# Optimization experiments

Hardware: AMD Instinct MI355X
Metric: run time of the kernel (lower is better)

The kernel has to match this reference:

```python
import jax, jax.numpy as jnp
import numpy as np

N = 8192
FEAT = 3
TRIG = 2
SA = 2
H = 64
ACT = 3
NEG = -1.0e9
EPS = 1e-5


def setup_inputs() -> dict:
    key = jax.random.key(0)
    ks = jax.random.split(key, 24)
    s = 0.05
    node_features = jax.random.uniform(ks[0], (N, FEAT), dtype=jnp.float32)
    adj = jax.random.randint(ks[1], (N, N), 0, 2).astype(jnp.float32)
    # ensure self-loops so every row has at least one neighbor
    adj_matrix = jnp.maximum(adj, jnp.eye(N, dtype=jnp.float32))
    trigger_context = jax.random.uniform(ks[2], (TRIG,), dtype=jnp.float32)
    sa_priors = jax.random.normal(ks[3], (N, SA), dtype=jnp.float32)
    p = lambda k, sh: jax.random.normal(k, sh, dtype=jnp.float32) * s
    return {
        "node_features": node_features,
        "adj_matrix": adj_matrix,
        "trigger_context": trigger_context,
        "sa_priors": sa_priors,
        # node_encoder: Linear(5,64) -> ReLU -> Linear(64,64)
        "w1": p(ks[4], (FEAT + TRIG, H)), "b1": jnp.zeros((H,), jnp.float32),
        "w2": p(ks[5], (H, H)), "b2": jnp.zeros((H,), jnp.float32),
        "wq": p(ks[6], (H, H)), "bq": jnp.zeros((H,), jnp.float32),
        "wk": p(ks[7], (H, H)), "bk": jnp.zeros((H,), jnp.float32),
        "wg": p(ks[8], (TRIG, H)), "bg": jnp.zeros((H,), jnp.float32),
        "stateful_bias": jnp.zeros((1,), jnp.float32),
        "wm": p(ks[9], (H, H)), "bm": jnp.zeros((H,), jnp.float32),
        "ln_g": jnp.ones((H,), jnp.float32), "ln_b": jnp.zeros((H,), jnp.float32),
        "wa1": p(ks[10], (H + SA, H)), "ba1": jnp.zeros((H,), jnp.float32),
        "wa2": p(ks[11], (H, ACT)), "ba2": jnp.zeros((ACT,), jnp.float32),
    }


def reference(node_features, adj_matrix, trigger_context, sa_priors,
              w1, b1, w2, b2, wq, bq, wk, bk, wg, bg, stateful_bias,
              wm, bm, ln_g, ln_b, wa1, ba1, wa2, ba2):
    n = node_features.shape[0]
    trig = jnp.broadcast_to(trigger_context[None, :], (n, TRIG))
    x = jnp.concatenate([node_features, trig], axis=1)          # [N, 5]
    h = jax.nn.relu(x @ w1 + b1) @ w2 + b2                       # [N, H]
    q = h @ wq + bq
    k = h @ wk + bk
    scores = (q @ k.T) * (1.0 / np.sqrt(H))                      # [N, N]
    gate_factor = jnp.mean(jax.nn.sigmoid(trigger_context @ wg + bg))
    topo = jnp.where(adj_matrix == 0, jnp.float32(NEG), adj_matrix)
    is_stateful = node_features[:, 2]
    is_reactive = 1.0 - trigger_context[0]
    sb = jnp.outer(is_stateful, is_stateful) * (stateful_bias[0] * is_reactive)
    scores = scores * gate_factor + topo + sb
    attn = jax.nn.softmax(scores, axis=1)                        # [N, N]
    messages = h @ wm + bm
    aggregated = attn @ messages                                 # [N, H]
    z = h + aggregated
    mu = jnp.mean(z, axis=-1, keepdims=True)
    var = jnp.mean(jnp.square(z - mu), axis=-1, keepdims=True)
    emb = (z - mu) * jax.lax.rsqrt(var + EPS) * ln_g + ln_b      # LayerNorm
    ai = jnp.concatenate([emb, sa_priors], axis=1)               # [N, H+2]
    q_values = jax.nn.relu(ai @ wa1 + ba1) @ wa2 + ba2           # [N, 3]
    return q_values
```

## Files before the change

kernel.cpp:

```cpp
#include <hip/hip_runtime.h>
#include <hip/hip_bf16.h>
#include <math.h>

#define N 8192
#define EPSV 1e-05f
#define NSPLIT 16
#define CPS (N / NSPLIT)
#define NTILE (CPS / 64)

typedef short bf16x8 __attribute__((ext_vector_type(8)));
typedef float f32x4 __attribute__((ext_vector_type(4)));
typedef float f32x16 __attribute__((ext_vector_type(16)));
typedef unsigned short u16;
typedef unsigned int u32;

#define WS_SCAL 0
#define WS_H    64
#define WS_ST   (WS_H + N * 64)
#define WS_SBI  (WS_ST + N)
#define WS_DEN  (WS_SBI + N)
#define WS_AGG  (WS_DEN + N)
#define WS_F_END (WS_AGG + N * 64)
#define WU_BASE (WS_F_END * 2)
#define WU_QB (WU_BASE)
#define WU_KB (WU_BASE + N * 64)
#define WU_MB (WU_BASE + 2 * N * 64)
#define WU_MT (WU_BASE + 3 * N * 64)

static __device__ __forceinline__ u16 f2bf(float f) {
    __hip_bfloat16 h = __float2bfloat16(f);
    return *(u16*)&h;
}
static __device__ __forceinline__ u32 pk2(float a, float b) {
    return (u32)f2bf(a) | ((u32)f2bf(b) << 16);
}
static __device__ __forceinline__ bf16x8 mk8(u32 a, u32 b, u32 c, u32 d) {
    union { u32 u[4]; bf16x8 v; } x;
    x.u[0] = a; x.u[1] = b; x.u[2] = c; x.u[3] = d;
    return x.v;
}

#define TILE_BARRIER() asm volatile("s_waitcnt lgkmcnt(0)\n\ts_barrier" ::: "memory")

__global__ void prep_k(const float* __restrict__ tc, const float* __restrict__ wg,
                       const float* __restrict__ bg, const float* __restrict__ sbias,
                       float* __restrict__ scal) {
    int j = threadIdx.x;
    float v = tc[0] * wg[j] + tc[1] * wg[64 + j] + bg[j];
    float g = 1.0f / (1.0f + __expf(-v));
    for (int off = 32; off; off >>= 1) g += __shfl_xor(g, off, 64);
    if (j == 0) {
        scal[0] = 0.125f * (g * (1.0f / 64.0f));
        scal[1] = sbias[0] * (1.0f - tc[0]);
    }
}

__global__ __launch_bounds__(256) void embed_k(
    const float* __restrict__ nf, const float* __restrict__ tc,
    const float* __restrict__ w1, const float* __restrict__ b1,
    const float* __restrict__ w2, const float* __restrict__ b2,
    const float* __restrict__ wq, const float* __restrict__ bq,
    const float* __restrict__ wk, const float* __restrict__ bk,
    const float* __restrict__ wm, const float* __restrict__ bm,
    float* __restrict__ ws)
{
    const int w = threadIdx.x >> 6, lane = threadIdx.x & 63;
    const int row = blockIdx.x * 4 + w;
    __shared__ float ts[4][64], hs[4][64];
    const float qscale = ws[WS_SCAL + 0];
    const float coef   = ws[WS_SCAL + 1];
    const float f0 = nf[row * 3], f1 = nf[row * 3 + 1], f2 = nf[row * 3 + 2];
    const float t0 = tc[0], t1 = tc[1];
    ws[WS_AGG + (size_t)row * 64 + lane] = 0.0f;
    float v = b1[lane];
    v = fmaf(f0, w1[lane], v);
    v = fmaf(f1, w1[64 + lane], v);
    v = fmaf(f2, w1[128 + lane], v);
    v = fmaf(t0, w1[192 + lane], v);
    v = fmaf(t1, w1[256 + lane], v);
    ts[w][lane] = fmaxf(v, 0.0f);
    __syncthreads();
    float hv = b2[lane];
    #pragma unroll 8
    for (int j = 0; j < 64; j++) hv = fmaf(ts[w][j], w2[j * 64 + lane], hv);
    hs[w][lane] = hv;
    ws[WS_H + row * 64 + lane] = hv;
    __syncthreads();
    float qv = bq[lane], kv = bk[lane], mv = bm[lane];
    #pragma unroll 4
    for (int j = 0; j < 64; j++) {
        const float hj = hs[w][j];
        qv = fmaf(hj, wq[j * 64 + lane], qv);
        kv = fmaf(hj, wk[j * 64 + lane], kv);
        mv = fmaf(hj, wm[j * 64 + lane], mv);
    }
    u16* wu = (u16*)ws;
    wu[WU_QB + row * 64 + lane] = f2bf(qv * qscale);
    wu[WU_KB + row * 64 + lane] = f2bf(kv);
    wu[WU_MB + row * 64 + lane] = f2bf(mv);
    if (lane == 0) {
        ws[WS_ST + row]  = f2;
        ws[WS_SBI + row] = f2 * coef;
        ws[WS_DEN + row] = 0.0f;
    }
}

__global__ __launch_bounds__(256) void transp_k(float* __restrict__ ws) {
    const u16* mb = (const u16*)ws + WU_MB;
    u16* mt = (u16*)ws + WU_MT;
    __shared__ __align__(16) u16 tile[64][72];
    const int i0 = blockIdx.x * 64;
    const int t = threadIdx.x;
    {
        const int r = t >> 2, cb = (t & 3) * 16;
        *(uint4*)&tile[r][cb]     = *(const uint4*)&mb[(size_t)(i0 + r) * 64 + cb];
        *(uint4*)&tile[r][cb + 8] = *(const uint4*)&mb[(size_t)(i0 + r) * 64 + cb + 8];
    }
    __syncthreads();
    const int c = t >> 2, rb = (t & 3) * 16;
    u16 tmp[16];
    #pragma unroll
    for (int i = 0; i < 16; i++) tmp[i] = tile[rb + i][c];
    *(uint4*)&mt[(size_t)c * N + i0 + rb]     = *(uint4*)&tmp[0];
    *(uint4*)&mt[(size_t)c * N + i0 + rb + 8] = *(uint4*)&tmp[8];
}

__global__ __launch_bounds__(256, 3) void attn_k(const float* __restrict__ adj,
                                                 float* __restrict__ ws)
{
    const int rb = blockIdx.x, sp = blockIdx.y;
    const int i0 = rb * 128, j0 = sp * CPS;
    const int tid = threadIdx.x;
    const int w = tid >> 6, lane = tid & 63;
    const int hi = lane >> 5, l31 = lane & 31;

    __shared__ __align__(16) u16 ks[2][64][68];
    __shared__ __align__(16) u16 ms[2][64][68];
    __shared__ float stl[CPS];

    const u16* qb  = (const u16*)ws + WU_QB;
    const u16* kbp = (const u16*)ws + WU_KB;
    const u16* mtp = (const u16*)ws + WU_MT;

    const int sr = tid >> 2, scb = (tid & 3) * 16;

    *(uint4*)&ks[0][sr][scb]     = *(const uint4*)&kbp[(size_t)(j0 + sr) * 64 + scb];
    *(uint4*)&ks[0][sr][scb + 8] = *(const uint4*)&kbp[(size_t)(j0 + sr) * 64 + scb + 8];
    *(uint4*)&ms[0][sr][scb]     = *(const uint4*)&mtp[(size_t)sr * N + j0 + scb];
    *(uint4*)&ms[0][sr][scb + 8] = *(const uint4*)&mtp[(size_t)sr * N + j0 + scb + 8];
    stl[tid]       = ws[WS_ST + j0 + tid];
    stl[tid + 256] = ws[WS_ST + j0 + tid + 256];
    __syncthreads();

    const int qrow = i0 + w * 32 + l31;
    const u16* qr = qb + (size_t)qrow * 64;
    bf16x8 qf[4];
    #pragma unroll
    for (int s = 0; s < 4; s++) qf[s] = *(const bf16x8*)&qr[s * 16 + hi * 8];

    const float sbr = ws[WS_SBI + qrow];
    const float* adjr = adj + (size_t)qrow * N;

    f32x16 acc[2];
    #pragma unroll
    for (int hb = 0; hb < 2; hb++)
        #pragma unroll
        for (int i = 0; i < 16; i++) acc[hb][i] = 0.0f;
    float den = 0.0f;

    f32x4 av[4];
    #pragma unroll
    for (int c2 = 0; c2 < 4; c2++)
        av[c2] = *(const f32x4*)&adjr[j0 + c2 * 8 + hi * 4];

    uint4 rk0, rk1, rm0, rm1;

    for (int t = 0; t < NTILE; t++) {
        const int cur = t & 1;
        #pragma unroll
        for (int kb = 0; kb < 2; kb++) {
            const int colb = j0 + t * 64 + kb * 32;
            const int loc  = t * 64 + kb * 32;

            if (kb == 0 && t + 1 < NTILE) {
                const int jn = j0 + (t + 1) * 64;
                rk0 = *(const uint4*)&kbp[(size_t)(jn + sr) * 64 + scb];
                rk1 = *(const uint4*)&kbp[(size_t)(jn + sr) * 64 + scb + 8];
                rm0 = *(const uint4*)&mtp[(size_t)sr * N + jn + scb];
                rm1 = *(const uint4*)&mtp[(size_t)sr * N + jn + scb + 8];
            }

            const bool pn = (2 * t + kb + 1 < 2 * NTILE);
            f32x4 avn[4];
            if (pn) {
                #pragma unroll
                for (int c2 = 0; c2 < 4; c2++)
                    avn[c2] = *(const f32x4*)&adjr[colb + 32 + c2 * 8 + hi * 4];
            } else {
                #pragma unroll
                for (int c2 = 0; c2 < 4; c2++) avn[c2] = av[c2];
            }

            f32x16 d;
            #pragma unroll
            for (int i = 0; i < 16; i++) d[i] = 0.0f;
            #pragma unroll
            for (int s = 0; s < 4; s++) {
                const bf16x8 kf = *(const bf16x8*)&ks[cur][kb * 32 + l31][s * 16 + hi * 8];
                d = __builtin_amdgcn_mfma_f32_32x32x16_bf16(kf, qf[s], d, 0, 0, 0);
            }

            u32 wlo[4], whi[4];
            #pragma unroll
            for (int c2 = 0; c2 < 4; c2++) {
                const f32x4 sv = *(const f32x4*)&stl[loc + c2 * 8 + hi * 4];
                const f32x4 a4 = av[c2];
                const float p0 = a4[0] * __expf(fmaf(sbr, sv[0], d[c2 * 4 + 0]));
                const float p1 = a4[1] * __expf(fmaf(sbr, sv[1], d[c2 * 4 + 1]));
                const float p2 = a4[2] * __expf(fmaf(sbr, sv[2], d[c2 * 4 + 2]));
                const float p3 = a4[3] * __expf(fmaf(sbr, sv[3], d[c2 * 4 + 3]));
                den += (p0 + p1) + (p2 + p3);
                wlo[c2] = pk2(p0, p1);
                whi[c2] = pk2(p2, p3);
            }

            bf16x8 pa[2];
            #pragma unroll
            for (int s2 = 0; s2 < 2; s2++) {
                const u32 xl0 = (u32)__shfl_xor((int)wlo[2 * s2],     32, 64);
                const u32 xh0 = (u32)__shfl_xor((int)whi[2 * s2],     32, 64);
                const u32 xl1 = (u32)__shfl_xor((int)wlo[2 * s2 + 1], 32, 64);
                const u32 xh1 = (u32)__shfl_xor((int)whi[2 * s2 + 1], 32, 64);
                const u32 f0 = hi ? xl1 : wlo[2 * s2];
                const u32 f1 = hi ? xh1 : whi[2 * s2];
                const u32 f2 = hi ? wlo[2 * s2 + 1] : xl0;
                const u32 f3 = hi ? whi[2 * s2 + 1] : xh0;
                pa[s2] = mk8(f0, f1, f2, f3);
            }

            #pragma unroll
            for (int hb = 0; hb < 2; hb++) {
                #pragma unroll
                for (int s2 = 0; s2 < 2; s2++) {
                    const bf16x8 mf = *(const bf16x8*)
                        &ms[cur][hb * 32 + l31][kb * 32 + s2 * 16 + hi * 8];
                    acc[hb] = __builtin_amdgcn_mfma_f32_32x32x16_bf16(pa[s2], mf, acc[hb], 0, 0, 0);
                }
            }

            if (kb == 1 && t + 1 < NTILE) {
                *(uint4*)&ks[cur ^ 1][sr][scb]     = rk0;
                *(uint4*)&ks[cur ^ 1][sr][scb + 8] = rk1;
                *(uint4*)&ms[cur ^ 1][sr][scb]     = rm0;
                *(uint4*)&ms[cur ^ 1][sr][scb + 8] = rm1;
            }

            #pragma unroll
            for (int c2 = 0; c2 < 4; c2++) av[c2] = avn[c2];
        }
        if (t + 1 < NTILE) TILE_BARRIER();
    }

    float* aggp = ws + WS_AGG;
    #pragma unroll
    for (int hb = 0; hb < 2; hb++) {
        #pragma unroll
        for (int reg = 0; reg < 16; reg++) {
            const int qv = (reg & 3) + 8 * (reg >> 2) + 4 * hi;
            unsafeAtomicAdd(&aggp[(size_t)(i0 + w * 32 + qv) * 64 + hb * 32 + l31],
                            acc[hb][reg]);
        }
    }
    den += __shfl_xor(den, 32, 64);
    if (hi == 0) unsafeAtomicAdd(&ws[WS_DEN + i0 + w * 32 + l31], den);
}

__global__ __launch_bounds__(256) void final_k(
    const float* __restrict__ sa, const float* __restrict__ ln_g,
    const float* __restrict__ ln_b,
    const float* __restrict__ wa1, const float* __restrict__ ba1,
    const float* __restrict__ wa2, const float* __restrict__ ba2,
    const float* __restrict__ ws, float* __restrict__ out)
{
    const int w = threadIdx.x >> 6, lane = threadIdx.x & 63;
    const int row = blockIdx.x * 4 + w;
    __shared__ float es[4][64], hs2[4][64];
    const float a = ws[WS_AGG + (size_t)row * 64 + lane];
    const float d = ws[WS_DEN + row];
    const float z = ws[WS_H + row * 64 + lane] + a / d;
    float mu = z;
    for (int off = 32; off; off >>= 1) mu += __shfl_xor(mu, off, 64);
    mu *= (1.0f / 64.0f);
    const float zc = z - mu;
    float var = zc * zc;
    for (int off = 32; off; off >>= 1) var += __shfl_xor(var, off, 64);
    var *= (1.0f / 64.0f);
    const float emb = zc * rsqrtf(var + EPSV) * ln_g[lane] + ln_b[lane];
    es[w][lane] = emb;
    __syncthreads();
    const float sa0 = sa[row * 2], sa1 = sa[row * 2 + 1];
    float hv = ba1[lane];
    #pragma unroll 8
    for (int c = 0; c < 64; c++) hv = fmaf(es[w][c], wa1[c * 64 + lane], hv);
    hv = fmaf(sa0, wa1[64 * 64 + lane], hv);
    hv = fmaf(sa1, wa1[65 * 64 + lane], hv);
    hs2[w][lane] = fmaxf(hv, 0.0f);
    __syncthreads();
    if (lane < 3) {
        float o = ba2[lane];
        for (int u = 0; u < 64; u++) o = fmaf(hs2[w][u], wa2[u * 3 + lane], o);
        out[row * 3 + lane] = o;
    }
}

extern "C" void kernel_launch(void* const* d_in, const int* in_sizes, int n_in,
                              void* d_out, int out_size, void* d_ws, size_t ws_size,
                              hipStream_t stream)
{
    const float* nf  = (const float*)d_in[0];
    const float* adj = (const float*)d_in[1];
    const float* tc  = (const float*)d_in[2];
    const float* sa  = (const float*)d_in[3];
    const float* w1  = (const float*)d_in[4];
    const float* b1  = (const float*)d_in[5];
    const float* w2  = (const float*)d_in[6];
    const float* b2  = (const float*)d_in[7];
    const float* wq  = (const float*)d_in[8];
    const float* bq  = (const float*)d_in[9];
    const float* wk  = (const float*)d_in[10];
    const float* bk  = (const float*)d_in[11];
    const float* wg  = (const float*)d_in[12];
    const float* bg  = (const float*)d_in[13];
    const float* sb  = (const float*)d_in[14];
    const float* wm  = (const float*)d_in[15];
    const float* bm  = (const float*)d_in[16];
    const float* lng = (const float*)d_in[17];
    const float* lnb = (const float*)d_in[18];
    const float* wa1 = (const float*)d_in[19];
    const float* ba1 = (const float*)d_in[20];
    const float* wa2 = (const float*)d_in[21];
    const float* ba2 = (const float*)d_in[22];
    float* ws  = (float*)d_ws;
    float* out = (float*)d_out;

    prep_k<<<1, 64, 0, stream>>>(tc, wg, bg, sb, ws + WS_SCAL);
    embed_k<<<N / 4, 256, 0, stream>>>(nf, tc, w1, b1, w2, b2, wq, bq, wk, bk,
                                       wm, bm, ws);
    transp_k<<<N / 64, 256, 0, stream>>>(ws);
    attn_k<<<dim3(N / 128, NSPLIT), 256, 0, stream>>>(adj, ws);
    final_k<<<N / 4, 256, 0, stream>>>(sa, lng, lnb, wa1, ba1, wa2, ba2, ws, out);
}
```

Measured before the change: 471.0 us.

## Transpose score MFMA output and stage probabilities through LDS instead of shuffles

Swaps the MFMA operand order so each lane holds one key column across 16 query rows. Adjacency loads become scalar per-row loads that are coalesced across lanes. Probabilities are written to a per-wave LDS tile and read back as bf16x8 operands, which replaces the cross-half shuffle repacking. The denominator is now reduced across lanes at the end. The costs are 16 scalar adj loads per step instead of four vector loads, extra LDS traffic, and higher register use for den and sbir, which may hurt occupancy.

```diff
diff --git a/kernel.cpp b/kernel.cpp
--- a/kernel.cpp
+++ b/kernel.cpp
@@ -30,14 +30,6 @@
 static __device__ __forceinline__ u16 f2bf(float f) {
     __hip_bfloat16 h = __float2bfloat16(f);
     return *(u16*)&h;
-}
-static __device__ __forceinline__ u32 pk2(float a, float b) {
-    return (u32)f2bf(a) | ((u32)f2bf(b) << 16);
-}
-static __device__ __forceinline__ bf16x8 mk8(u32 a, u32 b, u32 c, u32 d) {
-    union { u32 u[4]; bf16x8 v; } x;
-    x.u[0] = a; x.u[1] = b; x.u[2] = c; x.u[3] = d;
-    return x.v;
 }
 
 #define TILE_BARRIER() asm volatile("s_waitcnt lgkmcnt(0)\n\ts_barrier" ::: "memory")
@@ -136,6 +128,7 @@
 
     __shared__ __align__(16) u16 ks[2][64][68];
     __shared__ __align__(16) u16 ms[2][64][68];
+    __shared__ __align__(16) u16 ps[4][32][40];
     __shared__ float stl[CPS];
 
     const u16* qb  = (const u16*)ws + WU_QB;
@@ -152,26 +145,37 @@
     stl[tid + 256] = ws[WS_ST + j0 + tid + 256];
     __syncthreads();
 
-    const int qrow = i0 + w * 32 + l31;
-    const u16* qr = qb + (size_t)qrow * 64;
+    const int q0 = i0 + w * 32;
+
+    const u16* qr = qb + (size_t)(q0 + l31) * 64;
     bf16x8 qf[4];
     #pragma unroll
     for (int s = 0; s < 4; s++) qf[s] = *(const bf16x8*)&qr[s * 16 + hi * 8];
 
-    const float sbr = ws[WS_SBI + qrow];
-    const float* adjr = adj + (size_t)qrow * N;
+    float sbir[16];
+    #pragma unroll
+    for (int r = 0; r < 16; r++) {
+        const int qv = (r & 3) + 8 * (r >> 2) + 4 * hi;
+        sbir[r] = ws[WS_SBI + q0 + qv];
+    }
 
     f32x16 acc[2];
     #pragma unroll
     for (int hb = 0; hb < 2; hb++)
         #pragma unroll
         for (int i = 0; i < 16; i++) acc[hb][i] = 0.0f;
-    float den = 0.0f;
-
-    f32x4 av[4];
-    #pragma unroll
-    for (int c2 = 0; c2 < 4; c2++)
-        av[c2] = *(const f32x4*)&adjr[j0 + c2 * 8 + hi * 4];
+    float den[16];
+    #pragma unroll
+    for (int r = 0; r < 16; r++) den[r] = 0.0f;
+
+    const float* adjh = adj + (size_t)(q0 + 4 * hi) * N + j0 + l31;
+
+    float ac[16], an[16];
+    #pragma unroll
+    for (int r = 0; r < 16; r++) {
+        const int cr = (r & 3) + 8 * (r >> 2);
+        ac[r] = adjh[(size_t)cr * N];
+    }
 
     uint4 rk0, rk1, rm0, rm1;
 
@@ -179,8 +183,7 @@
         const int cur = t & 1;
         #pragma unroll
         for (int kb = 0; kb < 2; kb++) {
-            const int colb = j0 + t * 64 + kb * 32;
-            const int loc  = t * 64 + kb * 32;
+            const int loc = t * 64 + kb * 32;
 
             if (kb == 0 && t + 1 < NTILE) {
                 const int jn = j0 + (t + 1) * 64;
@@ -190,15 +193,15 @@
                 rm1 = *(const uint4*)&mtp[(size_t)sr * N + jn + scb + 8];
             }
 
-            const bool pn = (2 * t + kb + 1 < 2 * NTILE);
-            f32x4 avn[4];
-            if (pn) {
+            if (loc + 32 < CPS) {
                 #pragma unroll
-                for (int c2 = 0; c2 < 4; c2++)
-                    avn[c2] = *(const f32x4*)&adjr[colb + 32 + c2 * 8 + hi * 4];
+                for (int r = 0; r < 16; r++) {
+                    const int cr = (r & 3) + 8 * (r >> 2);
+                    an[r] = adjh[(size_t)cr * N + loc + 32];
+                }
             } else {
                 #pragma unroll
-                for (int c2 = 0; c2 < 4; c2++) avn[c2] = av[c2];
+                for (int r = 0; r < 16; r++) an[r] = ac[r];
             }
 
             f32x16 d;
@@ -207,44 +210,26 @@
             #pragma unroll
             for (int s = 0; s < 4; s++) {
                 const bf16x8 kf = *(const bf16x8*)&ks[cur][kb * 32 + l31][s * 16 + hi * 8];
-                d = __builtin_amdgcn_mfma_f32_32x32x16_bf16(kf, qf[s], d, 0, 0, 0);
-            }
-
-            u32 wlo[4], whi[4];
-            #pragma unroll
-            for (int c2 = 0; c2 < 4; c2++) {
-                const f32x4 sv = *(const f32x4*)&stl[loc + c2 * 8 + hi * 4];
-                const f32x4 a4 = av[c2];
-                const float p0 = a4[0] * __expf(fmaf(sbr, sv[0], d[c2 * 4 + 0]));
-                const float p1 = a4[1] * __expf(fmaf(sbr, sv[1], d[c2 * 4 + 1]));
-                const float p2 = a4[2] * __expf(fmaf(sbr, sv[2], d[c2 * 4 + 2]));
-                const float p3 = a4[3] * __expf(fmaf(sbr, sv[3], d[c2 * 4 + 3]));
-                den += (p0 + p1) + (p2 + p3);
-                wlo[c2] = pk2(p0, p1);
-                whi[c2] = pk2(p2, p3);
-            }
-
-            bf16x8 pa[2];
+                d = __builtin_amdgcn_mfma_f32_32x32x16_bf16(qf[s], kf, d, 0, 0, 0);
+            }
+
+            const float stc = stl[loc + l31];
+            #pragma unroll
+            for (int r = 0; r < 16; r++) {
+                const int qv = (r & 3) + 8 * (r >> 2) + 4 * hi;
+                const float p = ac[r] * __expf(fmaf(sbir[r], stc, d[r]));
+                den[r] += p;
+                ps[w][qv][l31] = f2bf(p);
+            }
+
             #pragma unroll
             for (int s2 = 0; s2 < 2; s2++) {
-                const u32 xl0 = (u32)__shfl_xor((int)wlo[2 * s2],     32, 64);
-                const u32 xh0 = (u32)__shfl_xor((int)whi[2 * s2],     32, 64);
-                const u32 xl1 = (u32)__shfl_xor((int)wlo[2 * s2 + 1], 32, 64);
-                const u32 xh1 = (u32)__shfl_xor((int)whi[2 * s2 + 1], 32, 64);
-                const u32 f0 = hi ? xl1 : wlo[2 * s2];
-                const u32 f1 = hi ? xh1 : whi[2 * s2];
-                const u32 f2 = hi ? wlo[2 * s2 + 1] : xl0;
-                const u32 f3 = hi ? whi[2 * s2 + 1] : xh0;
-                pa[s2] = mk8(f0, f1, f2, f3);
-            }
-
-            #pragma unroll
-            for (int hb = 0; hb < 2; hb++) {
+                const bf16x8 pa = *(const bf16x8*)&ps[w][l31][s2 * 16 + hi * 8];
                 #pragma unroll
-                for (int s2 = 0; s2 < 2; s2++) {
+                for (int hb = 0; hb < 2; hb++) {
                     const bf16x8 mf = *(const bf16x8*)
                         &ms[cur][hb * 32 + l31][kb * 32 + s2 * 16 + hi * 8];
-                    acc[hb] = __builtin_amdgcn_mfma_f32_32x32x16_bf16(pa[s2], mf, acc[hb], 0, 0, 0);
+                    acc[hb] = __builtin_amdgcn_mfma_f32_32x32x16_bf16(pa, mf, acc[hb], 0, 0, 0);
                 }
             }
 
@@ -256,23 +241,39 @@
             }
 
             #pragma unroll
-            for (int c2 = 0; c2 < 4; c2++) av[c2] = avn[c2];
+            for (int r = 0; r < 16; r++) ac[r] = an[r];
         }
         if (t + 1 < NTILE) TILE_BARRIER();
     }
 
+    #pragma unroll
+    for (int r = 0; r < 16; r++) {
+        float dv = den[r];
+        dv += __shfl_xor(dv, 1, 64);
+        dv += __shfl_xor(dv, 2, 64);
+        dv += __shfl_xor(dv, 4, 64);
+        dv += __shfl_xor(dv, 8, 64);
+        dv += __shfl_xor(dv, 16, 64);
+        den[r] = dv;
+    }
+    if (l31 == 0) {
+        #pragma unroll
+        for (int r = 0; r < 16; r++) {
+            const int qv = (r & 3) + 8 * (r >> 2) + 4 * hi;
+            unsafeAtomicAdd(&ws[WS_DEN + q0 + qv], den[r]);
+        }
+    }
+
     float* aggp = ws + WS_AGG;
     #pragma unroll
     for (int hb = 0; hb < 2; hb++) {
         #pragma unroll
-        for (int reg = 0; reg < 16; reg++) {
-            const int qv = (reg & 3) + 8 * (reg >> 2) + 4 * hi;
-            unsafeAtomicAdd(&aggp[(size_t)(i0 + w * 32 + qv) * 64 + hb * 32 + l31],
-                            acc[hb][reg]);
+        for (int r = 0; r < 16; r++) {
+            const int qv = (r & 3) + 8 * (r >> 2) + 4 * hi;
+            unsafeAtomicAdd(&aggp[(size_t)(q0 + qv) * 64 + hb * 32 + l31],
+                            acc[hb][r]);
         }
     }
-    den += __shfl_xor(den, 32, 64);
-    if (hi == 0) unsafeAtomicAdd(&ws[WS_DEN + i0 + w * 32 + l31], den);
 }
 
 __global__ __launch_bounds__(256) void final_k(
```

Result: no change. 474.5 us (+0.8%).

## Pre-pack Q/K/M into MFMA fragment layout and drop LDS staging in attention

Applied to the files above, without the earlier changes.

Replaces the transpose kernel with a pack kernel that writes Q, K and M into per-lane MFMA fragment order. The stateful-bias term is folded in as a fifth K-slice (sbi in Q, st in K), so the bias comes out of the QK MFMA instead of a separate fma. The attention kernel now reads fragments straight from global/L2 with no shared memory or barriers, doubles the column split to 32, prefetches adjacency two steps ahead, and raises wave priority around MFMA blocks. In exchange there is more L2 traffic per block, the bias is rounded to bf16, and twice as many atomic partial-sum writes.

```diff
diff --git a/kernel.cpp b/kernel.cpp
--- a/kernel.cpp
+++ b/kernel.cpp
@@ -4,9 +4,9 @@
 
 #define N 8192
 #define EPSV 1e-05f
-#define NSPLIT 16
+#define NSPLIT 32
 #define CPS (N / NSPLIT)
-#define NTILE (CPS / 64)
+#define NSTEP (CPS / 32)
 
 typedef short bf16x8 __attribute__((ext_vector_type(8)));
 typedef float f32x4 __attribute__((ext_vector_type(4)));
@@ -25,7 +25,9 @@
 #define WU_QB (WU_BASE)
 #define WU_KB (WU_BASE + N * 64)
 #define WU_MB (WU_BASE + 2 * N * 64)
-#define WU_MT (WU_BASE + 3 * N * 64)
+#define WU_QP (WU_BASE + 3 * N * 64)
+#define WU_KP (WU_QP + (N / 32) * 5 * 64 * 8)
+#define WU_MP (WU_KP + (N / 32) * 5 * 64 * 8)
 
 static __device__ __forceinline__ u16 f2bf(float f) {
     __hip_bfloat16 h = __float2bfloat16(f);
@@ -39,8 +41,6 @@
     x.u[0] = a; x.u[1] = b; x.u[2] = c; x.u[3] = d;
     return x.v;
 }
-
-#define TILE_BARRIER() asm volatile("s_waitcnt lgkmcnt(0)\n\ts_barrier" ::: "memory")
 
 __global__ void prep_k(const float* __restrict__ tc, const float* __restrict__ wg,
                        const float* __restrict__ bg, const float* __restrict__ sbias,
@@ -105,24 +105,42 @@
     }
 }
 
-__global__ __launch_bounds__(256) void transp_k(float* __restrict__ ws) {
-    const u16* mb = (const u16*)ws + WU_MB;
-    u16* mt = (u16*)ws + WU_MT;
-    __shared__ __align__(16) u16 tile[64][72];
-    const int i0 = blockIdx.x * 64;
-    const int t = threadIdx.x;
+__global__ __launch_bounds__(256) void pack_k(float* __restrict__ ws) {
+    const int b = blockIdx.x;
+    const int tid = threadIdx.x;
+    const int w = tid >> 6, lane = tid & 63;
+    const int hi = lane >> 5, l31 = lane & 31;
+    u16* wu = (u16*)ws;
+    const u16* qb = wu + WU_QB;
+    const u16* kb = wu + WU_KB;
+    const u16* mb = wu + WU_MB;
+
+    for (int s = w; s < 5; s += 4) {
+        uint4 vq, vk;
+        if (s < 4) {
+            vq = *(const uint4*)&qb[(size_t)(b * 32 + l31) * 64 + s * 16 + hi * 8];
+            vk = *(const uint4*)&kb[(size_t)(b * 32 + l31) * 64 + s * 16 + hi * 8];
+        } else {
+            vq = make_uint4(0, 0, 0, 0);
+            vk = make_uint4(0, 0, 0, 0);
+            if (hi == 0) {
+                vq.x = (u32)f2bf(ws[WS_SBI + b * 32 + l31]);
+                vk.x = (u32)f2bf(ws[WS_ST  + b * 32 + l31]);
+            }
+        }
+        *(uint4*)&wu[WU_QP + ((size_t)(b * 5 + s) * 64 + lane) * 8] = vq;
+        *(uint4*)&wu[WU_KP + ((size_t)(b * 5 + s) * 64 + lane) * 8] = vk;
+    }
     {
-        const int r = t >> 2, cb = (t & 3) * 16;
-        *(uint4*)&tile[r][cb]     = *(const uint4*)&mb[(size_t)(i0 + r) * 64 + cb];
-        *(uint4*)&tile[r][cb + 8] = *(const uint4*)&mb[(size_t)(i0 + r) * 64 + cb + 8];
-    }
-    __syncthreads();
-    const int c = t >> 2, rb = (t & 3) * 16;
-    u16 tmp[16];
-    #pragma unroll
-    for (int i = 0; i < 16; i++) tmp[i] = tile[rb + i][c];
-    *(uint4*)&mt[(size_t)c * N + i0 + rb]     = *(uint4*)&tmp[0];
-    *(uint4*)&mt[(size_t)c * N + i0 + rb + 8] = *(uint4*)&tmp[8];
+        const int s2 = w >> 1, hb = w & 1;
+        const int h = hb * 32 + l31;
+        u16 e[8];
+        #pragma unroll
+        for (int j = 0; j < 8; j++)
+            e[j] = mb[(size_t)(b * 32 + s2 * 16 + hi * 8 + j) * 64 + h];
+        *(uint4*)&wu[WU_MP + ((size_t)(b * 4 + s2 * 2 + hb) * 64 + lane) * 8] =
+            *(uint4*)&e[0];
+    }
 }
 
 __global__ __launch_bounds__(256, 3) void attn_k(const float* __restrict__ adj,
@@ -134,32 +152,18 @@
     const int w = tid >> 6, lane = tid & 63;
     const int hi = lane >> 5, l31 = lane & 31;
 
-    __shared__ __align__(16) u16 ks[2][64][68];
-    __shared__ __align__(16) u16 ms[2][64][68];
-    __shared__ float stl[CPS];
-
-    const u16* qb  = (const u16*)ws + WU_QB;
-    const u16* kbp = (const u16*)ws + WU_KB;
-    const u16* mtp = (const u16*)ws + WU_MT;
-
-    const int sr = tid >> 2, scb = (tid & 3) * 16;
-
-    *(uint4*)&ks[0][sr][scb]     = *(const uint4*)&kbp[(size_t)(j0 + sr) * 64 + scb];
-    *(uint4*)&ks[0][sr][scb + 8] = *(const uint4*)&kbp[(size_t)(j0 + sr) * 64 + scb + 8];
-    *(uint4*)&ms[0][sr][scb]     = *(const uint4*)&mtp[(size_t)sr * N + j0 + scb];
-    *(uint4*)&ms[0][sr][scb + 8] = *(const uint4*)&mtp[(size_t)sr * N + j0 + scb + 8];
-    stl[tid]       = ws[WS_ST + j0 + tid];
-    stl[tid + 256] = ws[WS_ST + j0 + tid + 256];
-    __syncthreads();
-
-    const int qrow = i0 + w * 32 + l31;
-    const u16* qr = qb + (size_t)qrow * 64;
-    bf16x8 qf[4];
-    #pragma unroll
-    for (int s = 0; s < 4; s++) qf[s] = *(const bf16x8*)&qr[s * 16 + hi * 8];
-
-    const float sbr = ws[WS_SBI + qrow];
-    const float* adjr = adj + (size_t)qrow * N;
+    const u16* wu = (const u16*)ws;
+    const u16* QP = wu + WU_QP;
+    const u16* KP = wu + WU_KP;
+    const u16* MP = wu + WU_MP;
+
+    const int q0 = i0 + w * 32;
+    const int qb32 = q0 >> 5;
+
+    bf16x8 qf[5];
+    #pragma unroll
+    for (int s = 0; s < 5; s++)
+        qf[s] = *(const bf16x8*)&QP[((size_t)(qb32 * 5 + s) * 64 + lane) * 8];
 
     f32x16 acc[2];
     #pragma unroll
@@ -168,111 +172,92 @@
         for (int i = 0; i < 16; i++) acc[hb][i] = 0.0f;
     float den = 0.0f;
 
-    f32x4 av[4];
-    #pragma unroll
-    for (int c2 = 0; c2 < 4; c2++)
-        av[c2] = *(const f32x4*)&adjr[j0 + c2 * 8 + hi * 4];
-
-    uint4 rk0, rk1, rm0, rm1;
-
-    for (int t = 0; t < NTILE; t++) {
-        const int cur = t & 1;
-        #pragma unroll
-        for (int kb = 0; kb < 2; kb++) {
-            const int colb = j0 + t * 64 + kb * 32;
-            const int loc  = t * 64 + kb * 32;
-
-            if (kb == 0 && t + 1 < NTILE) {
-                const int jn = j0 + (t + 1) * 64;
-                rk0 = *(const uint4*)&kbp[(size_t)(jn + sr) * 64 + scb];
-                rk1 = *(const uint4*)&kbp[(size_t)(jn + sr) * 64 + scb + 8];
-                rm0 = *(const uint4*)&mtp[(size_t)sr * N + jn + scb];
-                rm1 = *(const uint4*)&mtp[(size_t)sr * N + jn + scb + 8];
-            }
-
-            const bool pn = (2 * t + kb + 1 < 2 * NTILE);
-            f32x4 avn[4];
-            if (pn) {
-                #pragma unroll
-                for (int c2 = 0; c2 < 4; c2++)
-                    avn[c2] = *(const f32x4*)&adjr[colb + 32 + c2 * 8 + hi * 4];
-            } else {
-                #pragma unroll
-                for (int c2 = 0; c2 < 4; c2++) avn[c2] = av[c2];
-            }
-
-            f32x16 d;
-            #pragma unroll
-            for (int i = 0; i < 16; i++) d[i] = 0.0f;
-            #pragma unroll
-            for (int s = 0; s < 4; s++) {
-                const bf16x8 kf = *(const bf16x8*)&ks[cur][kb * 32 + l31][s * 16 + hi * 8];
-                d = __builtin_amdgcn_mfma_f32_32x32x16_bf16(kf, qf[s], d, 0, 0, 0);
-            }
-
-            u32 wlo[4], whi[4];
-            #pragma unroll
-            for (int c2 = 0; c2 < 4; c2++) {
-                const f32x4 sv = *(const f32x4*)&stl[loc + c2 * 8 + hi * 4];
-                const f32x4 a4 = av[c2];
-                const float p0 = a4[0] * __expf(fmaf(sbr, sv[0], d[c2 * 4 + 0]));
-                const float p1 = a4[1] * __expf(fmaf(sbr, sv[1], d[c2 * 4 + 1]));
-                const float p2 = a4[2] * __expf(fmaf(sbr, sv[2], d[c2 * 4 + 2]));
-                const float p3 = a4[3] * __expf(fmaf(sbr, sv[3], d[c2 * 4 + 3]));
-                den += (p0 + p1) + (p2 + p3);
-                wlo[c2] = pk2(p0, p1);
-                whi[c2] = pk2(p2, p3);
-            }
-
-            bf16x8 pa[2];
-            #pragma unroll
-            for (int s2 = 0; s2 < 2; s2++) {
-                const u32 xl0 = (u32)__shfl_xor((int)wlo[2 * s2],     32, 64);
-                const u32 xh0 = (u32)__shfl_xor((int)whi[2 * s2],     32, 64);
-                const u32 xl1 = (u32)__shfl_xor((int)wlo[2 * s2 + 1], 32, 64);
-                const u32 xh1 = (u32)__shfl_xor((int)whi[2 * s2 + 1], 32, 64);
-                const u32 f0 = hi ? xl1 : wlo[2 * s2];
-                const u32 f1 = hi ? xh1 : whi[2 * s2];
-                const u32 f2 = hi ? wlo[2 * s2 + 1] : xl0;
-                const u32 f3 = hi ? whi[2 * s2 + 1] : xh0;
-                pa[s2] = mk8(f0, f1, f2, f3);
-            }
-
+    const float* adjr = adj + (size_t)(q0 + l31) * N;
+    f32x4 av[4], avn[4];
+    #pragma unroll
+    for (int c2 = 0; c2 < 4; c2++) {
+        av[c2]  = *(const f32x4*)&adjr[j0 + c2 * 8 + hi * 4];
+        avn[c2] = *(const f32x4*)&adjr[j0 + 32 + c2 * 8 + hi * 4];
+    }
+
+    #pragma unroll
+    for (int s = 0; s < NSTEP; s++) {
+        const int kb = (j0 >> 5) + s;
+
+        const int pl = (s + 2 < NSTEP) ? j0 + s * 32 + 64 : j0 + s * 32;
+        f32x4 a2[4];
+        #pragma unroll
+        for (int c2 = 0; c2 < 4; c2++)
+            a2[c2] = *(const f32x4*)&adjr[pl + c2 * 8 + hi * 4];
+
+        f32x16 d;
+        #pragma unroll
+        for (int i = 0; i < 16; i++) d[i] = 0.0f;
+        __builtin_amdgcn_s_setprio(1);
+        #pragma unroll
+        for (int sl = 0; sl < 5; sl++) {
+            const bf16x8 kf = *(const bf16x8*)
+                &KP[((size_t)(kb * 5 + sl) * 64 + lane) * 8];
+            d = __builtin_amdgcn_mfma_f32_32x32x16_bf16(kf, qf[sl], d, 0, 0, 0);
+        }
+        __builtin_amdgcn_s_setprio(0);
+
+        u32 wlo[4], whi[4];
+        #pragma unroll
+        for (int c2 = 0; c2 < 4; c2++) {
+            const f32x4 a4 = av[c2];
+            const float p0 = a4[0] * __expf(d[c2 * 4 + 0]);
+            const float p1 = a4[1] * __expf(d[c2 * 4 + 1]);
+            const float p2 = a4[2] * __expf(d[c2 * 4 + 2]);
+            const float p3 = a4[3] * __expf(d[c2 * 4 + 3]);
+            den += (p0 + p1) + (p2 + p3);
+            wlo[c2] = pk2(p0, p1);
+            whi[c2] = pk2(p2, p3);
+        }
+
+        bf16x8 pa[2];
+        #pragma unroll
+        for (int s2 = 0; s2 < 2; s2++) {
+            const u32 xl0 = (u32)__shfl_xor((int)wlo[2 * s2],     32, 64);
+            const u32 xh0 = (u32)__shfl_xor((int)whi[2 * s2],     32, 64);
+            const u32 xl1 = (u32)__shfl_xor((int)wlo[2 * s2 + 1], 32, 64);
+            const u32 xh1 = (u32)__shfl_xor((int)whi[2 * s2 + 1], 32, 64);
+            const u32 f0 = hi ? xl1 : wlo[2 * s2];
+            const u32 f1 = hi ? xh1 : whi[2 * s2];
+            const u32 f2 = hi ? wlo[2 * s2 + 1] : xl0;
+            const u32 f3 = hi ? whi[2 * s2 + 1] : xh0;
+            pa[s2] = mk8(f0, f1, f2, f3);
+        }
+
+        __builtin_amdgcn_s_setprio(1);
+        #pragma unroll
+        for (int s2 = 0; s2 < 2; s2++) {
             #pragma unroll
             for (int hb = 0; hb < 2; hb++) {
-                #pragma unroll
-                for (int s2 = 0; s2 < 2; s2++) {
-                    const bf16x8 mf = *(const bf16x8*)
-                        &ms[cur][hb * 32 + l31][kb * 32 + s2 * 16 + hi * 8];
-                    acc[hb] = __builtin_amdgcn_mfma_f32_32x32x16_bf16(pa[s2], mf, acc[hb], 0, 0, 0);
-                }
+                const bf16x8 mf = *(const bf16x8*)
+                    &MP[((size_t)(kb * 4 + s2 * 2 + hb) * 64 + lane) * 8];
+                acc[hb] = __builtin_amdgcn_mfma_f32_32x32x16_bf16(pa[s2], mf, acc[hb], 0, 0, 0);
             }
-
-            if (kb == 1 && t + 1 < NTILE) {
-                *(uint4*)&ks[cur ^ 1][sr][scb]     = rk0;
-                *(uint4*)&ks[cur ^ 1][sr][scb + 8] = rk1;
-                *(uint4*)&ms[cur ^ 1][sr][scb]     = rm0;
-                *(uint4*)&ms[cur ^ 1][sr][scb + 8] = rm1;
-            }
-
-            #pragma unroll
-            for (int c2 = 0; c2 < 4; c2++) av[c2] = avn[c2];
-        }
-        if (t + 1 < NTILE) TILE_BARRIER();
-    }
+        }
+        __builtin_amdgcn_s_setprio(0);
+
+        #pragma unroll
+        for (int c2 = 0; c2 < 4; c2++) { av[c2] = avn[c2]; avn[c2] = a2[c2]; }
+    }
+
+    den += __shfl_xor(den, 32, 64);
+    if (hi == 0) unsafeAtomicAdd(&ws[WS_DEN + q0 + l31], den);
 
     float* aggp = ws + WS_AGG;
     #pragma unroll
     for (int hb = 0; hb < 2; hb++) {
         #pragma unroll
-        for (int reg = 0; reg < 16; reg++) {
-            const int qv = (reg & 3) + 8 * (reg >> 2) + 4 * hi;
-            unsafeAtomicAdd(&aggp[(size_t)(i0 + w * 32 + qv) * 64 + hb * 32 + l31],
-                            acc[hb][reg]);
-        }
-    }
-    den += __shfl_xor(den, 32, 64);
-    if (hi == 0) unsafeAtomicAdd(&ws[WS_DEN + i0 + w * 32 + l31], den);
+        for (int r = 0; r < 16; r++) {
+            const int qv = (r & 3) + 8 * (r >> 2) + 4 * hi;
+            unsafeAtomicAdd(&aggp[(size_t)(q0 + qv) * 64 + hb * 32 + l31],
+                            acc[hb][r]);
+        }
+    }
 }
 
 __global__ __launch_bounds__(256) void final_k(
@@ -346,7 +331,7 @@
     prep_k<<<1, 64, 0, stream>>>(tc, wg, bg, sb, ws + WS_SCAL);
     embed_k<<<N / 4, 256, 0, stream>>>(nf, tc, w1, b1, w2, b2, wq, bq, wk, bk,
                                        wm, bm, ws);
-    transp_k<<<N / 64, 256, 0, stream>>>(ws);
+    pack_k<<<N / 32, 256, 0, stream>>>(ws);
     attn_k<<<dim3(N / 128, NSPLIT), 256, 0, stream>>>(adj, ws);
     final_k<<<N / 4, 256, 0, stream>>>(sa, lng, lnb, wa1, ba1, wa2, ba2, ws, out);
 }
```

New measurement: 484.5 us. +2.9%, slower.
